# Kernel tuning notes

Measured on AMD Instinct MI355X. Metric: run time of the kernel, lower is better.

The kernel has to match this reference:

```python
import jax, jax.numpy as jnp
import numpy as np

NUM_HEADS = 8
HEAD_DIM = 64
HIDDEN_SIZE = 128
TOP_K = 16
EPS = 1e-6


def setup_inputs() -> dict:
    key = jax.random.key(0)
    k1, k2, k3 = jax.random.split(key, 3)
    B, H, S, D = 4, NUM_HEADS, 1024, HEAD_DIM
    return {
        "keys": jax.random.normal(k1, (B, H, S, D), dtype=jnp.float32),
        "values": jax.random.normal(k2, (B, H, S, D), dtype=jnp.float32),
        "queries": jax.random.normal(k3, (B, H, S, D), dtype=jnp.float32),
    }


def _project(x):
    # replicate [B,H,S,D] along last dim to cover HIDDEN_SIZE basis indices
    D = x.shape[-1]
    if D >= HIDDEN_SIZE:
        return x[..., :HIDDEN_SIZE]
    repeats = (HIDDEN_SIZE + D - 1) // D
    return jnp.tile(x, (1, 1, 1, repeats))[..., :HIDDEN_SIZE]


def reference(keys, values, queries):
    B, H, S, D = keys.shape
    b_idx = jnp.arange(B)[:, None, None]   # [B,1,1]
    h_idx = jnp.arange(H)[None, :, None]   # [1,H,1]

    # ---- update: scatter-add outer products into assigned memory bank ----
    assignments = jnp.argmax(jnp.abs(_project(keys)), axis=-1)  # [B,H,S]
    outer = values[..., :, None] * keys[..., None, :]           # [B,H,S,D,D] (v k^T)
    M = jnp.zeros((B, H, HIDDEN_SIZE, D, D), dtype=keys.dtype)
    M = M.at[b_idx, h_idx, assignments].add(outer)
    z = jnp.zeros((B, H, HIDDEN_SIZE, D), dtype=keys.dtype)
    z = z.at[b_idx, h_idx, assignments].add(keys)

    # ---- retrieve: top-k basis selection, gather-matvec, weighted combine ----
    scores = jnp.abs(_project(queries))                          # [B,H,S,HIDDEN]
    top_scores, top_idx = jax.lax.top_k(scores, TOP_K)           # [B,H,S,K]
    weights = jax.nn.softmax(top_scores, axis=-1)

    output = jnp.zeros((B, H, S, D), dtype=queries.dtype)
    for k in range(TOP_K):
        mem = top_idx[..., k]                                    # [B,H,S]
        M_sel = M[b_idx, h_idx, mem]                             # [B,H,S,D,D]
        z_sel = z[b_idx, h_idx, mem]                             # [B,H,S,D]
        num = jnp.einsum('bhsde,bhse->bhsd', M_sel, queries)
        den = jnp.einsum('bhsd,bhsd->bhs', z_sel, queries)[..., None] + EPS
        output = output + weights[..., k:k + 1] * (num / den)
    return output
```

## Files before the change

### kernel.cpp

```cpp
#include <hip/hip_runtime.h>
#include <math.h>

#define S_LEN 1024
#define EPS 1e-6f

typedef __attribute__((ext_vector_type(8)))  short bf16x8;
typedef __attribute__((ext_vector_type(16))) float float16v;


__device__ __forceinline__ void wave_argmax(float& bv, int& bi) {
    #pragma unroll
    for (int off = 1; off < 64; off <<= 1) {
        float ov = __shfl_xor(bv, off, 64);
        int   oi = __shfl_xor(bi, off, 64);
        if (ov > bv || (ov == bv && oi < bi)) { bv = ov; bi = oi; }
    }
}

__device__ __forceinline__ unsigned short f2bf(float f) {
    unsigned int u = __float_as_uint(f);
    unsigned int r = (u + 0x7fffu + ((u >> 16) & 1u)) >> 16;
    return (unsigned short)r;
}

__device__ __forceinline__ bf16x8 pack8(float4 a, float4 b) {
    bf16x8 r;
    r[0] = (short)f2bf(a.x); r[1] = (short)f2bf(a.y);
    r[2] = (short)f2bf(a.z); r[3] = (short)f2bf(a.w);
    r[4] = (short)f2bf(b.x); r[5] = (short)f2bf(b.y);
    r[6] = (short)f2bf(b.z); r[7] = (short)f2bf(b.w);
    return r;
}

__global__ __launch_bounds__(256) void k_pre(const float* __restrict__ keys,
                                             const float* __restrict__ queries,
                                             int* __restrict__ kcnt2,
                                             unsigned short* __restrict__ klist2,
                                             int* __restrict__ qcnt2,
                                             unsigned* __restrict__ qpair,
                                             float* __restrict__ out) {
    const int bh   = blockIdx.x >> 5;
    const int blk  = blockIdx.x & 31;
    const int wv   = threadIdx.x >> 6;
    const int lane = threadIdx.x & 63;

    __shared__ int khist[64], qhist[64];
    if (threadIdx.x < 64) { khist[threadIdx.x] = 0; qhist[threadIdx.x] = 0; }
    __syncthreads();

    const int s0 = blk * 32 + wv * 8;
    float kv[8], qv[8];
    #pragma unroll
    for (int i = 0; i < 8; ++i) {
        kv[i] = keys   [((size_t)bh * 1024 + s0 + i) * 64 + lane];
        qv[i] = queries[((size_t)bh * 1024 + s0 + i) * 64 + lane];
    }

    {
        float4 zz = {0.f, 0.f, 0.f, 0.f};
        float4* po = (float4*)(out + (size_t)blockIdx.x * 2048);
        po[threadIdx.x] = zz; po[threadIdx.x + 256] = zz;
    }

    #pragma unroll
    for (int i = 0; i < 8; ++i) {
        float bv = fabsf(kv[i]); int bi = lane;
        wave_argmax(bv, bi);
        if (lane == 0) {
            int pos = atomicAdd(&khist[bi], 1);
            klist2[((size_t)bh * 64 + bi) * 1024 + blk * 32 + pos] =
                (unsigned short)(s0 + i);
        }
    }

    #pragma unroll
    for (int i = 0; i < 8; ++i) {
        unsigned ud = __float_as_uint(qv[i]) & 0x7fffffffu;
        int gt = 0;
        #pragma unroll
        for (int k = 0; k < 64; ++k) {
            unsigned ui = (unsigned)__builtin_amdgcn_readlane((int)ud, k);
            gt += (ui > ud) ? 1 : 0;
        }
        int S = gt;
        #pragma unroll
        for (int off = 1; off < 64; off <<= 1) S += __shfl_xor(S, off, 64);
        float e = expf(__uint_as_float(ud));
        int copies, contrib;
        if (S == 2016) {
            contrib = (gt < 8);
            copies  = contrib ? 2 : 0;
        } else {
            int eq = 0, eql = 0;
            #pragma unroll
            for (int k = 0; k < 64; ++k) {
                unsigned ui = (unsigned)__builtin_amdgcn_readlane((int)ud, k);
                eq  += (ui == ud) ? 1 : 0;
                eql += (ui == ud && k < lane) ? 1 : 0;
            }
            int pos_low  = 2 * gt + eql;
            int pos_high = pos_low + eq;
            copies  = (pos_low < 16 ? 1 : 0) + (pos_high < 16 ? 1 : 0);
            contrib = (pos_low < 16);
        }
        float ce = (float)copies * e;
        #pragma unroll
        for (int off = 1; off < 64; off <<= 1) ce += __shfl_xor(ce, off, 64);
        if (contrib) {
            int pos = atomicAdd(&qhist[lane], 1);
            unsigned wb = __float_as_uint(e / ce) & 0xFFFFFC00u;
            qpair[((size_t)bh * 64 + lane) * 1024 + blk * 32 + pos] =
                wb | (unsigned)(s0 + i);
        }
    }
    __syncthreads();
    if (threadIdx.x < 64) {
        kcnt2[(bh * 32 + blk) * 64 + threadIdx.x] = khist[threadIdx.x];
        qcnt2[(bh * 32 + blk) * 64 + threadIdx.x] = qhist[threadIdx.x];
    }
}

__global__ __launch_bounds__(256) void k_main(const float* __restrict__ keys,
                                              const float* __restrict__ values,
                                              const float* __restrict__ queries,
                                              const int* __restrict__ kcnt2,
                                              const unsigned short* __restrict__ klist2,
                                              const int* __restrict__ qcnt2,
                                              const unsigned* __restrict__ qpair,
                                              float* __restrict__ out) {
    const int bh    = blockIdx.x & 31;
    const int bank  = blockIdx.x >> 5;
    const int t     = threadIdx.x;
    const int lane  = t & 63;
    const int grp   = t >> 6;

    __shared__ alignas(16) unsigned short M_bf[64 * 64];
    __shared__ alignas(16) unsigned short Q_bf[64 * 64];
    __shared__ alignas(16) float Ou[64 * 66];
    __shared__ unsigned short s_match[1024];
    __shared__ unsigned q_ent[256];
    __shared__ int    koffs_s[33], qoffs_s[33];
    __shared__ float  z_s[64];
    __shared__ double den_s[64];
    __shared__ float  w_s[2][64];
    __shared__ int    sq_s[2][64];

    if (t < 64) {
        int i = t & 31;
        int c = (t < 32) ? kcnt2[(bh * 32 + i) * 64 + bank]
                         : qcnt2[(bh * 32 + i) * 64 + bank];
        #pragma unroll
        for (int off = 1; off < 32; off <<= 1) {
            int o = __shfl(c, t - off, 64);
            if (i >= off) c += o;
        }
        if (t < 32) { if (i == 0) koffs_s[0] = 0; koffs_s[i + 1] = c; }
        else        { if (i == 0) qoffs_s[0] = 0; qoffs_s[i + 1] = c; }
    }
    __syncthreads();

    const int nm = koffs_s[32];
    const int nq = qoffs_s[32];
    if (nm == 0 || nq == 0) return;

    for (int idx = t; idx < nm; idx += 256) {
        int seg = 0;
        #pragma unroll
        for (int i = 1; i < 32; ++i) if (idx >= koffs_s[i]) seg = i;
        s_match[idx] = klist2[(size_t)(bh * 64 + bank) * 1024 + seg * 32 +
                              (idx - koffs_s[seg])];
    }
    __syncthreads();

    float acc[16];
    #pragma unroll
    for (int m = 0; m < 16; ++m) acc[m] = 0.f;
    float zacc = 0.f;
    const float* kb = keys   + (size_t)bh * S_LEN * 64;
    const float* vb = values + (size_t)bh * S_LEN * 64;
    for (int base = 0, it = 0; base < nm; base += 8, ++it) {
        float* kst = Ou + (it & 1) * 1024;
        float* vst = kst + 512;
        #pragma unroll
        for (int rr = 0; rr < 2; ++rr) {
            int row = grp + rr * 4;
            if (base + row < nm) {
                int s = s_match[base + row];
                kst[row * 64 + lane] = kb[(size_t)s * 64 + lane];
                vst[row * 64 + lane] = vb[(size_t)s * 64 + lane];
            }
        }
        __syncthreads();
        int lim = min(8, nm - base);
        for (int jj = 0; jj < lim; ++jj) {
            float kv = kst[jj * 64 + lane];
            #pragma unroll
            for (int m = 0; m < 16; ++m)
                acc[m] += vst[jj * 64 + grp * 16 + m] * kv;
        }
        if (t < 64)
            for (int jj = 0; jj < lim; ++jj) zacc += kst[jj * 64 + t];
    }
    #pragma unroll
    for (int m = 0; m < 16; ++m) {
        int dv = grp * 16 + m;
        M_bf[dv * 64 + (((lane >> 3) ^ (dv & 7)) << 3) + (lane & 7)] = f2bf(acc[m]);
    }
    if (t < 64) z_s[t] = zacc;

    const float* qb = queries + (size_t)bh * S_LEN * 64;
    float*       ob = out     + (size_t)bh * S_LEN * 64;
    const int dvh = grp >> 1, jh = grp & 1;

    int prev_nb = 0;
    for (int qbase = 0, batch = 0; qbase < nq; qbase += 64, ++batch) {
        const int nb  = min(64, nq - qbase);
        const int cur = batch & 1;

        if ((qbase & 255) == 0) {
            if (qbase + t < nq) {
                int jg = qbase + t;
                int seg = 0;
                #pragma unroll
                for (int i = 1; i < 32; ++i) if (jg >= qoffs_s[i]) seg = i;
                q_ent[t] = qpair[(size_t)(bh * 64 + bank) * 1024 + seg * 32 +
                                 (jg - qoffs_s[seg])];
            }
            __syncthreads();
        }

        if (batch > 0) {
            #pragma unroll
            for (int jj = 0; jj < 16; ++jj) {
                int j = grp * 16 + jj;
                if (j < prev_nb) {
                    float v = Ou[j * 66 + lane];
                    unsafeAtomicAdd(&ob[(size_t)sq_s[1 - cur][j] * 64 + lane], v);
                }
            }
        }
        {
            int j = t >> 2, c4 = t & 3;
            bf16x8 p0 = {}, p1 = {};
            double d = 0.0;
            if (j < nb) {
                unsigned e = q_ent[(qbase & 255) + j];
                int s = (int)(e & 1023u);
                if ((t & 3) == 0) {
                    sq_s[cur][j] = s;
                    w_s[cur][j]  = __uint_as_float(e & 0xFFFFFC00u);
                }
                const float4* src = (const float4*)(qb + (size_t)s * 64 + c4 * 16);
                float4 f0 = src[0], f1 = src[1], f2 = src[2], f3 = src[3];
                p0 = pack8(f0, f1);
                p1 = pack8(f2, f3);
                const float4* zz4 = (const float4*)&z_s[c4 * 16];
                float4 z0 = zz4[0], z1 = zz4[1], z2 = zz4[2], z3 = zz4[3];
                d  = (double)z0.x * f0.x + (double)z0.y * f0.y + (double)z0.z * f0.z + (double)z0.w * f0.w;
                d += (double)z1.x * f1.x + (double)z1.y * f1.y + (double)z1.z * f1.z + (double)z1.w * f1.w;
                d += (double)z2.x * f2.x + (double)z2.y * f2.y + (double)z2.z * f2.z + (double)z2.w * f2.w;
                d += (double)z3.x * f3.x + (double)z3.y * f3.y + (double)z3.z * f3.z + (double)z3.w * f3.w;
            }
            int c0 = c4 * 2;
            *(bf16x8*)&Q_bf[j * 64 + ((c0 ^ (j & 7)) << 3)]       = p0;
            *(bf16x8*)&Q_bf[j * 64 + (((c0 + 1) ^ (j & 7)) << 3)] = p1;
            d += __shfl_xor(d, 1, 64);
            d += __shfl_xor(d, 2, 64);
            if ((t & 3) == 0) den_s[j] = d;
        }
        __syncthreads();

        float16v C;
        #pragma unroll
        for (int i = 0; i < 16; ++i) C[i] = 0.f;
        const int am = dvh * 32 + (lane & 31);
        const int bn = jh  * 32 + (lane & 31);
        #pragma unroll
        for (int ks = 0; ks < 4; ++ks) {
            int ch = ks * 2 + (lane >> 5);
            bf16x8 af = *(const bf16x8*)&M_bf[am * 64 + ((ch ^ (am & 7)) << 3)];
            bf16x8 bf = *(const bf16x8*)&Q_bf[bn * 64 + ((ch ^ (bn & 7)) << 3)];
            C = __builtin_amdgcn_mfma_f32_32x32x16_bf16(af, bf, C, 0, 0, 0);
        }
        {
            double den = den_s[bn];
            float  w   = w_s[cur][bn];
            float rinv = (float)((double)w / (den + (double)EPS));
            #pragma unroll
            for (int r = 0; r < 16; ++r) {
                int dv = dvh * 32 + (r & 3) + 8 * (r >> 2) + 4 * (lane >> 5);
                Ou[bn * 66 + dv] = C[r] * rinv;
            }
        }
        __syncthreads();
        prev_nb = nb;
    }
    {
        const int cur = (((nq + 63) >> 6) - 1) & 1;
        #pragma unroll
        for (int jj = 0; jj < 16; ++jj) {
            int j = grp * 16 + jj;
            if (j < prev_nb) {
                float v = Ou[j * 66 + lane];
                unsafeAtomicAdd(&ob[(size_t)sq_s[cur][j] * 64 + lane], v);
            }
        }
    }
}

extern "C" void kernel_launch(void* const* d_in, const int* in_sizes, int n_in,
                              void* d_out, int out_size, void* d_ws, size_t ws_size,
                              hipStream_t stream) {
    const float* keys    = (const float*)d_in[0];
    const float* values  = (const float*)d_in[1];
    const float* queries = (const float*)d_in[2];
    char* ws = (char*)d_ws;
    int*            kcnt2  = (int*)(ws);
    int*            qcnt2  = (int*)(ws + 262144);
    unsigned short* klist2 = (unsigned short*)(ws + 524288);
    unsigned*       qpair  = (unsigned*)(ws + 4718592);

    k_pre <<<1024, 256, 0, stream>>>(keys, queries, kcnt2, klist2, qcnt2, qpair,
                                     (float*)d_out);
    k_main<<<2048, 256, 0, stream>>>(keys, values, queries, kcnt2, klist2, qcnt2, qpair,
                                     (float*)d_out);
}
```

Before: 162.0 us.

## Make retrieval phase wave-independent with per-wave query chunks and register B fragments

The query retrieval loop is restructured so that each wave independently processes 32-query chunks. Each wave loads query rows straight from global memory into bf16 MFMA B fragments in registers, computes the denominator with a lane shuffle, and runs two MFMAs to cover all 64 output dims. Results are staged in a small per-wave LDS tile before the atomic adds. This removes the block-wide __syncthreads, the shared Q_bf/Ou staging and the batch double-buffering of the old 64-query loop. In exchange, every lane redoes the segment search and the qpair load, and a block with few chunks can leave waves idle.

```diff
diff --git a/kernel.cpp b/kernel.cpp
--- a/kernel.cpp
+++ b/kernel.cpp
@@ -135,15 +135,10 @@
     const int grp   = t >> 6;
 
     __shared__ alignas(16) unsigned short M_bf[64 * 64];
-    __shared__ alignas(16) unsigned short Q_bf[64 * 64];
-    __shared__ alignas(16) float Ou[64 * 66];
+    __shared__ alignas(16) float Tq[4 * 16 * 68];
     __shared__ unsigned short s_match[1024];
-    __shared__ unsigned q_ent[256];
-    __shared__ int    koffs_s[33], qoffs_s[33];
-    __shared__ float  z_s[64];
-    __shared__ double den_s[64];
-    __shared__ float  w_s[2][64];
-    __shared__ int    sq_s[2][64];
+    __shared__ int   koffs_s[33], qoffs_s[33];
+    __shared__ float z_s[64];
 
     if (t < 64) {
         int i = t & 31;
@@ -179,7 +174,7 @@
     const float* kb = keys   + (size_t)bh * S_LEN * 64;
     const float* vb = values + (size_t)bh * S_LEN * 64;
     for (int base = 0, it = 0; base < nm; base += 8, ++it) {
-        float* kst = Ou + (it & 1) * 1024;
+        float* kst = Tq + (it & 1) * 1024;
         float* vst = kst + 512;
         #pragma unroll
         for (int rr = 0; rr < 2; ++rr) {
@@ -207,102 +202,77 @@
         M_bf[dv * 64 + (((lane >> 3) ^ (dv & 7)) << 3) + (lane & 7)] = f2bf(acc[m]);
     }
     if (t < 64) z_s[t] = zacc;
+    __syncthreads();
 
     const float* qb = queries + (size_t)bh * S_LEN * 64;
     float*       ob = out     + (size_t)bh * S_LEN * 64;
-    const int dvh = grp >> 1, jh = grp & 1;
-
-    int prev_nb = 0;
-    for (int qbase = 0, batch = 0; qbase < nq; qbase += 64, ++batch) {
-        const int nb  = min(64, nq - qbase);
-        const int cur = batch & 1;
-
-        if ((qbase & 255) == 0) {
-            if (qbase + t < nq) {
-                int jg = qbase + t;
-                int seg = 0;
+    float* tile = Tq + grp * (16 * 68);
+
+    const int j32 = lane & 31;
+    const int h   = lane >> 5;
+    const int nchunks = (nq + 31) >> 5;
+    for (int c = grp; c < nchunks; c += 4) {
+        const int cbase = c * 32;
+        const int rem = min(32, nq - cbase);
+        int jg = cbase + ((j32 < rem) ? j32 : (rem - 1));
+        int seg = 0;
+        #pragma unroll
+        for (int i = 1; i < 32; ++i) if (jg >= qoffs_s[i]) seg = i;
+        unsigned e = qpair[(size_t)(bh * 64 + bank) * 1024 + seg * 32 +
+                           (jg - qoffs_s[seg])];
+        int   s = (int)(e & 1023u);
+        float w = (j32 < rem) ? __uint_as_float(e & 0xFFFFFC00u) : 0.f;
+
+        const float* qrow = qb + (size_t)s * 64 + h * 8;
+        bf16x8 bfrag[4];
+        double den = 0.0;
+        #pragma unroll
+        for (int ks = 0; ks < 4; ++ks) {
+            const float4* p = (const float4*)(qrow + ks * 16);
+            float4 f0 = p[0], f1 = p[1];
+            bfrag[ks] = pack8(f0, f1);
+            const float4* zp = (const float4*)(z_s + ks * 16 + h * 8);
+            float4 z0 = zp[0], z1 = zp[1];
+            den += (double)z0.x * f0.x + (double)z0.y * f0.y
+                 + (double)z0.z * f0.z + (double)z0.w * f0.w
+                 + (double)z1.x * f1.x + (double)z1.y * f1.y
+                 + (double)z1.z * f1.z + (double)z1.w * f1.w;
+        }
+        den += __shfl_xor(den, 32, 64);
+
+        float16v C0, C1;
+        #pragma unroll
+        for (int i = 0; i < 16; ++i) { C0[i] = 0.f; C1[i] = 0.f; }
+        #pragma unroll
+        for (int ks = 0; ks < 4; ++ks) {
+            int ch = ks * 2 + h;
+            int a0r = j32, a1r = 32 + j32;
+            bf16x8 a0 = *(const bf16x8*)&M_bf[a0r * 64 + ((ch ^ (a0r & 7)) << 3)];
+            bf16x8 a1 = *(const bf16x8*)&M_bf[a1r * 64 + ((ch ^ (a1r & 7)) << 3)];
+            C0 = __builtin_amdgcn_mfma_f32_32x32x16_bf16(a0, bfrag[ks], C0, 0, 0, 0);
+            C1 = __builtin_amdgcn_mfma_f32_32x32x16_bf16(a1, bfrag[ks], C1, 0, 0, 0);
+        }
+        float rinv = (float)((double)w / (den + (double)EPS));
+
+        #pragma unroll
+        for (int pass = 0; pass < 2; ++pass) {
+            if ((j32 >> 4) == pass) {
+                int row = j32 & 15;
                 #pragma unroll
-                for (int i = 1; i < 32; ++i) if (jg >= qoffs_s[i]) seg = i;
-                q_ent[t] = qpair[(size_t)(bh * 64 + bank) * 1024 + seg * 32 +
-                                 (jg - qoffs_s[seg])];
-            }
-            __syncthreads();
-        }
-
-        if (batch > 0) {
-            #pragma unroll
-            for (int jj = 0; jj < 16; ++jj) {
-                int j = grp * 16 + jj;
-                if (j < prev_nb) {
-                    float v = Ou[j * 66 + lane];
-                    unsafeAtomicAdd(&ob[(size_t)sq_s[1 - cur][j] * 64 + lane], v);
+                for (int rq = 0; rq < 4; ++rq) {
+                    float4 v0 = { C0[rq * 4 + 0] * rinv, C0[rq * 4 + 1] * rinv,
+                                  C0[rq * 4 + 2] * rinv, C0[rq * 4 + 3] * rinv };
+                    float4 v1 = { C1[rq * 4 + 0] * rinv, C1[rq * 4 + 1] * rinv,
+                                  C1[rq * 4 + 2] * rinv, C1[rq * 4 + 3] * rinv };
+                    *(float4*)&tile[row * 68 + rq * 8 + h * 4]      = v0;
+                    *(float4*)&tile[row * 68 + 32 + rq * 8 + h * 4] = v1;
                 }
             }
-        }
-        {
-            int j = t >> 2, c4 = t & 3;
-            bf16x8 p0 = {}, p1 = {};
-            double d = 0.0;
-            if (j < nb) {
-                unsigned e = q_ent[(qbase & 255) + j];
-                int s = (int)(e & 1023u);
-                if ((t & 3) == 0) {
-                    sq_s[cur][j] = s;
-                    w_s[cur][j]  = __uint_as_float(e & 0xFFFFFC00u);
-                }
-                const float4* src = (const float4*)(qb + (size_t)s * 64 + c4 * 16);
-                float4 f0 = src[0], f1 = src[1], f2 = src[2], f3 = src[3];
-                p0 = pack8(f0, f1);
-                p1 = pack8(f2, f3);
-                const float4* zz4 = (const float4*)&z_s[c4 * 16];
-                float4 z0 = zz4[0], z1 = zz4[1], z2 = zz4[2], z3 = zz4[3];
-                d  = (double)z0.x * f0.x + (double)z0.y * f0.y + (double)z0.z * f0.z + (double)z0.w * f0.w;
-                d += (double)z1.x * f1.x + (double)z1.y * f1.y + (double)z1.z * f1.z + (double)z1.w * f1.w;
-                d += (double)z2.x * f2.x + (double)z2.y * f2.y + (double)z2.z * f2.z + (double)z2.w * f2.w;
-                d += (double)z3.x * f3.x + (double)z3.y * f3.y + (double)z3.z * f3.z + (double)z3.w * f3.w;
-            }
-            int c0 = c4 * 2;
-            *(bf16x8*)&Q_bf[j * 64 + ((c0 ^ (j & 7)) << 3)]       = p0;
-            *(bf16x8*)&Q_bf[j * 64 + (((c0 + 1) ^ (j & 7)) << 3)] = p1;
-            d += __shfl_xor(d, 1, 64);
-            d += __shfl_xor(d, 2, 64);
-            if ((t & 3) == 0) den_s[j] = d;
-        }
-        __syncthreads();
-
-        float16v C;
-        #pragma unroll
-        for (int i = 0; i < 16; ++i) C[i] = 0.f;
-        const int am = dvh * 32 + (lane & 31);
-        const int bn = jh  * 32 + (lane & 31);
-        #pragma unroll
-        for (int ks = 0; ks < 4; ++ks) {
-            int ch = ks * 2 + (lane >> 5);
-            bf16x8 af = *(const bf16x8*)&M_bf[am * 64 + ((ch ^ (am & 7)) << 3)];
-            bf16x8 bf = *(const bf16x8*)&Q_bf[bn * 64 + ((ch ^ (bn & 7)) << 3)];
-            C = __builtin_amdgcn_mfma_f32_32x32x16_bf16(af, bf, C, 0, 0, 0);
-        }
-        {
-            double den = den_s[bn];
-            float  w   = w_s[cur][bn];
-            float rinv = (float)((double)w / (den + (double)EPS));
-            #pragma unroll
-            for (int r = 0; r < 16; ++r) {
-                int dv = dvh * 32 + (r & 3) + 8 * (r >> 2) + 4 * (lane >> 5);
-                Ou[bn * 66 + dv] = C[r] * rinv;
-            }
-        }
-        __syncthreads();
-        prev_nb = nb;
-    }
-    {
-        const int cur = (((nq + 63) >> 6) - 1) & 1;
-        #pragma unroll
-        for (int jj = 0; jj < 16; ++jj) {
-            int j = grp * 16 + jj;
-            if (j < prev_nb) {
-                float v = Ou[j * 66 + lane];
-                unsafeAtomicAdd(&ob[(size_t)sq_s[cur][j] * 64 + lane], v);
+            int qrows = min(16, rem - pass * 16);
+            for (int jj = 0; jj < qrows; ++jj) {
+                int sj = __shfl(s, pass * 16 + jj, 64);
+                float v = tile[jj * 68 + lane];
+                unsafeAtomicAdd(&ob[(size_t)sj * 64 + lane], v);
             }
         }
     }
```

New measurement: 167.1 us. 3.2% more time.
